# Optimization experiments

Hardware: AMD Instinct MI355X
Metric: run time of the kernel (lower is better)

The kernel has to match this reference:

```python
import jax, jax.numpy as jnp
import numpy as np


def exp_mix_frac(p1, p2, a1, b1, a2, b2):
    # stable merge of two (numerator, denominator) pairs carried in log-scale p
    p = jnp.maximum(p1, p2)
    e1 = jnp.exp(p1 - p)
    e2 = jnp.exp(p2 - p)
    return a1 * e1 + a2 * e2, b1 * e1 + b2 * e2, p


def assoc_reduce_step(left, right):
    akv_l, ak_l, w_l, p_l = left
    akv_r, ak_r, w_r, p_r = right
    a, b, p = exp_mix_frac(p_l + w_r, p_r, akv_l, ak_l, akv_r, ak_r)
    return a, b, w_l + w_r, p


def setup_inputs() -> dict:
    key = jax.random.key(0)
    ks = jax.random.split(key, 7)
    S, B, E = 2048, 8, 1024
    scale = 1.0 / np.sqrt(E)
    return {
        "x": jax.random.normal(ks[0], (S, B, E), jnp.float32),
        "tmrkv": jax.random.uniform(ks[1], (3 * E,), jnp.float32),
        "Wk": jax.random.normal(ks[2], (E, E), jnp.float32) * scale,
        "Wv": jax.random.normal(ks[3], (E, E), jnp.float32) * scale,
        "time_decay": jax.random.normal(ks[4], (E,), jnp.float32) - 1.0,
        "time_first": jax.random.normal(ks[5], (E,), jnp.float32),
        "Wout": jax.random.normal(ks[6], (E, E), jnp.float32) * scale,
    }


def reference(x, tmrkv, Wk, Wv, time_decay, time_first, Wout):
    # x: (S, B, E) time-major (batch_first=False path of the source module)
    S, B, E = x.shape
    x_prev = jnp.concatenate([jnp.zeros_like(x[:1]), x[:-1]], axis=0)
    # time_mix_rkv layout: [r | k | v]; r-branch is computed in the source but
    # never used in the associative-scan path, so it is omitted (same output).
    mk = tmrkv[E:2 * E]
    mv = tmrkv[2 * E:]
    k = (mk * x + (1.0 - mk) * x_prev) @ Wk  # (S, B, E)
    v = (mv * x + (1.0 - mv) * x_prev) @ Wv  # (S, B, E)

    k_ = k.reshape(S, B * E)
    v_ = v.reshape(S, B * E)
    W_ = jnp.broadcast_to(jnp.tile(time_decay, B)[None, :], (S, B * E))
    ones = jnp.ones_like(v_)
    # log-depth parallel scan over time with numerically-stable exp merge
    a_, b_, _, p_ = jax.lax.associative_scan(
        assoc_reduce_step, (v_, ones, W_, k_), axis=0)

    a_state = a_.reshape(S, B, E)
    b_state = b_.reshape(S, B, E)
    p_state = p_.reshape(S, B, E)
    c, d, _ = exp_mix_frac(p_state, k + time_first + time_decay,
                           a_state, b_state, v, jnp.ones_like(v))
    rwkv = c / d  # (S, B, E)
    return rwkv @ Wout
```

## Files before the change

### kernel.cpp

```cpp
#include <hip/hip_runtime.h>
#include <stdint.h>

#define S_LEN  2048
#define B_DIM  8
#define E_DIM  1024
#define BE     (B_DIM * E_DIM)
#define M_ROWS (S_LEN * B_DIM)
#define NCHUNK 64
#define CLEN   (S_LEN / NCHUNK)

typedef __attribute__((ext_vector_type(8))) short bf16x8;
typedef __attribute__((ext_vector_type(4))) float f32x4;

__device__ __forceinline__ unsigned short f2bf(float f) {
    unsigned int u = __float_as_uint(f);
    u += 0x7FFFu + ((u >> 16) & 1u);
    return (unsigned short)(u >> 16);
}
__device__ __forceinline__ float bf_lo(unsigned int u) {
    return __uint_as_float(u << 16);
}
__device__ __forceinline__ float bf_hi(unsigned int u) {
    return __uint_as_float(u & 0xFFFF0000u);
}

__global__ __launch_bounds__(256) void mix_kernel(
    const float* __restrict__ x, const float* __restrict__ tmrkv,
    unsigned short* __restrict__ xk, unsigned short* __restrict__ xv)
{
    int i = blockIdx.x * 256 + threadIdx.x;
    const float4* x4 = (const float4*)x;
    float4 xc = x4[i];
    float4 xp = make_float4(0.f, 0.f, 0.f, 0.f);
    if (i >= BE / 4) xp = x4[i - BE / 4];
    int e4 = i & (E_DIM / 4 - 1);
    float4 mk = ((const float4*)(tmrkv + E_DIM))[e4];
    float4 mv = ((const float4*)(tmrkv + 2 * E_DIM))[e4];
    ushort4 ok, ov;
    ok.x = f2bf(mk.x * xc.x + (1.f - mk.x) * xp.x);
    ok.y = f2bf(mk.y * xc.y + (1.f - mk.y) * xp.y);
    ok.z = f2bf(mk.z * xc.z + (1.f - mk.z) * xp.z);
    ok.w = f2bf(mk.w * xc.w + (1.f - mk.w) * xp.w);
    ov.x = f2bf(mv.x * xc.x + (1.f - mv.x) * xp.x);
    ov.y = f2bf(mv.y * xc.y + (1.f - mv.y) * xp.y);
    ov.z = f2bf(mv.z * xc.z + (1.f - mv.z) * xp.z);
    ov.w = f2bf(mv.w * xc.w + (1.f - mv.w) * xp.w);
    ((ushort4*)xk)[i] = ok;
    ((ushort4*)xv)[i] = ov;
}

__global__ __launch_bounds__(256) void cast_transpose_k(
    const float* __restrict__ w0, const float* __restrict__ w1,
    const float* __restrict__ w2,
    unsigned short* __restrict__ o0, unsigned short* __restrict__ o1,
    unsigned short* __restrict__ o2)
{
    const float* in = blockIdx.z == 0 ? w0 : (blockIdx.z == 1 ? w1 : w2);
    unsigned short* out = blockIdx.z == 0 ? o0 : (blockIdx.z == 1 ? o1 : o2);
    __shared__ float tile[32][33];
    int bx = blockIdx.x * 32, by = blockIdx.y * 32;
    int tx = threadIdx.x, ty = threadIdx.y;
    #pragma unroll
    for (int i = 0; i < 32; i += 8)
        tile[ty + i][tx] = in[(size_t)(by + ty + i) * E_DIM + bx + tx];
    __syncthreads();
    #pragma unroll
    for (int i = 0; i < 32; i += 8)
        out[(size_t)(bx + ty + i) * E_DIM + by + tx] = f2bf(tile[tx][ty + i]);
}

#define BM 128
#define BN 128
#define BK 64

template <typename OutT>
__global__ __launch_bounds__(256) void gemm_bf16_bt(
    const unsigned short* __restrict__ A,
    const unsigned short* __restrict__ BT,
    OutT* __restrict__ C, int M, int N, int K)
{
    __shared__ __align__(16) unsigned short As[BM * BK];
    __shared__ __align__(16) unsigned short Bs[BN * BK];
    const int tid  = threadIdx.x;
    const int wave = tid >> 6, lane = tid & 63;
    const int bm = blockIdx.x * BM, bn = blockIdx.y * BN;
    const int wr = (wave >> 1) * 64, wc = (wave & 1) * 64;
    const int lrow = lane & 15, lq = lane >> 4;

    f32x4 acc[4][4];
    #pragma unroll
    for (int i = 0; i < 4; ++i)
        #pragma unroll
        for (int j = 0; j < 4; ++j)
            acc[i][j] = (f32x4){0.f, 0.f, 0.f, 0.f};

    const int nk = K / BK;
    for (int kt = 0; kt < nk; ++kt) {
        __syncthreads();
        const int kk = kt * BK;
        #pragma unroll
        for (int s = 0; s < 4; ++s) {
            int idx = s * 256 + wave * 64 + lane;
            int r   = idx >> 3;
            int gc  = (idx & 7) ^ (r & 7);
            const char* ga = (const char*)(A  + (size_t)(bm + r) * K + kk) + gc * 16;
            const char* gb = (const char*)(BT + (size_t)(bn + r) * K + kk) + gc * 16;
            char* la = (char*)As + s * 4096 + wave * 1024;
            char* lb = (char*)Bs + s * 4096 + wave * 1024;
            __builtin_amdgcn_global_load_lds(
                (const __attribute__((address_space(1))) unsigned int*)ga,
                (__attribute__((address_space(3))) unsigned int*)la, 16, 0, 0);
            __builtin_amdgcn_global_load_lds(
                (const __attribute__((address_space(1))) unsigned int*)gb,
                (__attribute__((address_space(3))) unsigned int*)lb, 16, 0, 0);
        }
        __syncthreads();

        #pragma unroll
        for (int h = 0; h < 2; ++h) {
            bf16x8 af[4], bf[4];
            #pragma unroll
            for (int i = 0; i < 4; ++i) {
                int R = wr + i * 16 + lrow;
                af[i] = *(const bf16x8*)&As[R * BK + (((h << 2) | lq) ^ (R & 7)) * 8];
            }
            #pragma unroll
            for (int j = 0; j < 4; ++j) {
                int R = wc + j * 16 + lrow;
                bf[j] = *(const bf16x8*)&Bs[R * BK + (((h << 2) | lq) ^ (R & 7)) * 8];
            }
            #pragma unroll
            for (int i = 0; i < 4; ++i)
                #pragma unroll
                for (int j = 0; j < 4; ++j)
                    acc[i][j] = __builtin_amdgcn_mfma_f32_16x16x32_bf16(
                        af[i], bf[j], acc[i][j], 0, 0, 0);
        }
    }

    #pragma unroll
    for (int i = 0; i < 4; ++i)
        #pragma unroll
        for (int j = 0; j < 4; ++j)
            #pragma unroll
            for (int r = 0; r < 4; ++r) {
                int row = bm + wr + i * 16 + lq * 4 + r;
                int col = bn + wc + j * 16 + lrow;
                if constexpr (sizeof(OutT) == 2)
                    C[(size_t)row * N + col] = f2bf(acc[i][j][r]);
                else
                    C[(size_t)row * N + col] = acc[i][j][r];
            }
}

__device__ __forceinline__ void wkv_step(float& a, float& b, float& p,
                                         float kt, float vt, float w)
{
    float pw = p + w;
    float pn = fmaxf(pw, kt);
    float e1 = __expf(pw - pn), e2 = __expf(kt - pn);
    a = a * e1 + vt * e2;
    b = b * e1 + e2;
    p = pn;
}

__global__ __launch_bounds__(256) void scan_pass1(
    const unsigned int* __restrict__ k2, const unsigned int* __restrict__ v2,
    const float* __restrict__ tdec,
    float2* __restrict__ sA, float2* __restrict__ sB, float2* __restrict__ sP)
{
    int g   = blockIdx.x * 256 + threadIdx.x;
    int ch2 = g & (BE / 2 - 1);
    int c   = g >> 12;
    float2 w2 = ((const float2*)tdec)[ch2 & (E_DIM / 2 - 1)];
    size_t idx = (size_t)c * CLEN * (BE / 2) + ch2;
    unsigned int ku = k2[idx], vu = v2[idx];
    float a0 = bf_lo(vu), b0 = 1.f, p0 = bf_lo(ku);
    float a1 = bf_hi(vu), b1 = 1.f, p1 = bf_hi(ku);
    for (int j = 1; j < CLEN; ++j) {
        idx += BE / 2;
        ku = k2[idx]; vu = v2[idx];
        wkv_step(a0, b0, p0, bf_lo(ku), bf_lo(vu), w2.x);
        wkv_step(a1, b1, p1, bf_hi(ku), bf_hi(vu), w2.y);
    }
    sA[g] = make_float2(a0, a1);
    sB[g] = make_float2(b0, b1);
    sP[g] = make_float2(p0, p1);
}

__global__ __launch_bounds__(256) void scan_pass2(
    const float* __restrict__ tdec,
    float* __restrict__ sA, float* __restrict__ sB, float* __restrict__ sP)
{
    __shared__ float tA[64 * 65], tB[64 * 65], tP[64 * 65];
    const int t   = threadIdx.x;
    const int ch0 = blockIdx.x * 64;
    const int chl = t & 63;
    const int cq  = t >> 6;
    #pragma unroll 4
    for (int cc = 0; cc < 16; ++cc) {
        int c = cq * 16 + cc;
        int idx = c * BE + ch0 + chl;
        tA[chl * 65 + c] = sA[idx];
        tB[chl * 65 + c] = sB[idx];
        tP[chl * 65 + c] = sP[idx];
    }
    __syncthreads();
    const int lane = t & 63, wave = t >> 6;
    for (int i = 0; i < 16; ++i) {
        int ch = wave * 16 + i;
        float w = tdec[(ch0 + ch) & (E_DIM - 1)];
        float a = tA[ch * 65 + lane];
        float b = tB[ch * 65 + lane];
        float p = tP[ch * 65 + lane];
        float W = (float)CLEN * w;
        #pragma unroll
        for (int d = 1; d < 64; d <<= 1) {
            float a_l = __shfl_up(a, d);
            float b_l = __shfl_up(b, d);
            float p_l = __shfl_up(p, d);
            float W_l = __shfl_up(W, d);
            if (lane >= d) {
                float pw = p_l + W;
                float pn = fmaxf(pw, p);
                float e1 = __expf(pw - pn), e2 = __expf(p - pn);
                a = a_l * e1 + a * e2;
                b = b_l * e1 + b * e2;
                p = pn;
                W = W_l + W;
            }
        }
        float ea = __shfl_up(a, 1);
        float eb = __shfl_up(b, 1);
        float ep = __shfl_up(p, 1);
        if (lane == 0) { ea = 0.f; eb = 0.f; ep = -__builtin_inff(); }
        tA[ch * 65 + lane] = ea;
        tB[ch * 65 + lane] = eb;
        tP[ch * 65 + lane] = ep;
    }
    __syncthreads();
    #pragma unroll 4
    for (int cc = 0; cc < 16; ++cc) {
        int c = cq * 16 + cc;
        int idx = c * BE + ch0 + chl;
        sA[idx] = tA[chl * 65 + c];
        sB[idx] = tB[chl * 65 + c];
        sP[idx] = tP[chl * 65 + c];
    }
}

__global__ __launch_bounds__(256) void scan_pass3(
    const unsigned int* __restrict__ k2, const unsigned int* __restrict__ v2,
    const float* __restrict__ tdec, const float* __restrict__ tfir,
    const float2* __restrict__ sA, const float2* __restrict__ sB,
    const float2* __restrict__ sP, unsigned int* __restrict__ rwkv2)
{
    int g   = blockIdx.x * 256 + threadIdx.x;
    int ch2 = g & (BE / 2 - 1);
    int c   = g >> 12;
    int e2  = ch2 & (E_DIM / 2 - 1);
    float2 w2 = ((const float2*)tdec)[e2];
    float2 f2 = ((const float2*)tfir)[e2];
    float u20 = f2.x + w2.x, u21 = f2.y + w2.y;
    float2 av = sA[g], bv = sB[g], pv = sP[g];
    float a0 = av.x, b0 = bv.x, p0 = pv.x;
    float a1 = av.y, b1 = bv.y, p1 = pv.y;
    size_t idx = (size_t)c * CLEN * (BE / 2) + ch2;
    for (int j = 0; j < CLEN; ++j) {
        unsigned int ku = k2[idx], vu = v2[idx];
        float kt0 = bf_lo(ku), vt0 = bf_lo(vu);
        float kt1 = bf_hi(ku), vt1 = bf_hi(vu);
        wkv_step(a0, b0, p0, kt0, vt0, w2.x);
        wkv_step(a1, b1, p1, kt1, vt1, w2.y);
        float kb0 = kt0 + u20, kb1 = kt1 + u21;
        float q0 = fmaxf(p0, kb0), q1 = fmaxf(p1, kb1);
        float g0 = __expf(p0 - q0), h0 = __expf(kb0 - q0);
        float g1 = __expf(p1 - q1), h1 = __expf(kb1 - q1);
        float r0 = (a0 * g0 + vt0 * h0) / (b0 * g0 + h0);
        float r1 = (a1 * g1 + vt1 * h1) / (b1 * g1 + h1);
        rwkv2[idx] = (unsigned int)f2bf(r0) | ((unsigned int)f2bf(r1) << 16);
        idx += BE / 2;
    }
}

extern "C" void kernel_launch(void* const* d_in, const int* in_sizes, int n_in,
                              void* d_out, int out_size, void* d_ws, size_t ws_size,
                              hipStream_t stream)
{
    const float* x     = (const float*)d_in[0];
    const float* tmrkv = (const float*)d_in[1];
    const float* Wk    = (const float*)d_in[2];
    const float* Wv    = (const float*)d_in[3];
    const float* tdec  = (const float*)d_in[4];
    const float* tfir  = (const float*)d_in[5];
    const float* Wout  = (const float*)d_in[6];
    float* out = (float*)d_out;

    char* ws = (char*)d_ws;
    const size_t SZ_BF = (size_t)M_ROWS * E_DIM * 2;
    unsigned short* xk   = (unsigned short*)(ws);
    unsigned short* xv   = (unsigned short*)(ws + SZ_BF);
    unsigned short* kbuf = (unsigned short*)(ws + 2 * SZ_BF);
    unsigned short* vbuf = (unsigned short*)(ws + 3 * SZ_BF);
    unsigned short* WkT  = (unsigned short*)(ws + 4 * SZ_BF);
    unsigned short* WvT  = WkT + (size_t)E_DIM * E_DIM;
    unsigned short* WoutT= WvT + (size_t)E_DIM * E_DIM;
    float* sA = (float*)xv;
    float* sB = sA + (size_t)NCHUNK * BE;
    float* sP = sB + (size_t)NCHUNK * BE;
    unsigned short* rwkv = xk;

    mix_kernel<<<(M_ROWS * E_DIM / 4) / 256, 256, 0, stream>>>(x, tmrkv, xk, xv);

    dim3 tb(32, 8), tg(E_DIM / 32, E_DIM / 32, 3);
    cast_transpose_k<<<tg, tb, 0, stream>>>(Wk, Wv, Wout, WkT, WvT, WoutT);

    dim3 gg(M_ROWS / BM, E_DIM / BN);
    gemm_bf16_bt<unsigned short><<<gg, 256, 0, stream>>>(xk, WkT, kbuf,
                                                         M_ROWS, E_DIM, E_DIM);
    gemm_bf16_bt<unsigned short><<<gg, 256, 0, stream>>>(xv, WvT, vbuf,
                                                         M_ROWS, E_DIM, E_DIM);

    scan_pass1<<<(NCHUNK * BE / 2) / 256, 256, 0, stream>>>(
        (const unsigned int*)kbuf, (const unsigned int*)vbuf, tdec,
        (float2*)sA, (float2*)sB, (float2*)sP);
    scan_pass2<<<BE / 64, 256, 0, stream>>>(tdec, sA, sB, sP);
    scan_pass3<<<(NCHUNK * BE / 2) / 256, 256, 0, stream>>>(
        (const unsigned int*)kbuf, (const unsigned int*)vbuf, tdec, tfir,
        (const float2*)sA, (const float2*)sB, (const float2*)sP,
        (unsigned int*)rwkv);

    gemm_bf16_bt<float><<<gg, 256, 0, stream>>>(rwkv, WoutT, out,
                                                M_ROWS, E_DIM, E_DIM);
}
```

Measured before the change: 337.0 us.

## Double scan chunks, merge K/V GEMMs, single-exp merges, widen mix kernel

Raises the scan chunk count to 128, which shortens each thread's serial chain and doubles scan-pass parallelism. The chunk-level prefix in pass2 now handles two chunks per lane. The K and V GEMMs become one launch with a z-dimension, and the GEMM grid is reordered so N varies fastest. Each stable exp merge now uses one exp of -|d| plus selects instead of two exps, and the output division uses a fast reciprocal. The mix kernel processes 8 elements per thread and the scan loops are unrolled. The cost is larger scan-state buffers and a slightly less precise division.

Result: no change. 332.9 us (-1.2%).

```diff
diff --git a/kernel.cpp b/kernel.cpp
--- a/kernel.cpp
+++ b/kernel.cpp
@@ -6,8 +6,9 @@
 #define E_DIM  1024
 #define BE     (B_DIM * E_DIM)
 #define M_ROWS (S_LEN * B_DIM)
-#define NCHUNK 64
+#define NCHUNK 128
 #define CLEN   (S_LEN / NCHUNK)
+#define P_PER_T (BE / 2)
 
 typedef __attribute__((ext_vector_type(8))) short bf16x8;
 typedef __attribute__((ext_vector_type(4))) float f32x4;
@@ -30,23 +31,35 @@
 {
     int i = blockIdx.x * 256 + threadIdx.x;
     const float4* x4 = (const float4*)x;
-    float4 xc = x4[i];
-    float4 xp = make_float4(0.f, 0.f, 0.f, 0.f);
-    if (i >= BE / 4) xp = x4[i - BE / 4];
-    int e4 = i & (E_DIM / 4 - 1);
-    float4 mk = ((const float4*)(tmrkv + E_DIM))[e4];
-    float4 mv = ((const float4*)(tmrkv + 2 * E_DIM))[e4];
-    ushort4 ok, ov;
-    ok.x = f2bf(mk.x * xc.x + (1.f - mk.x) * xp.x);
-    ok.y = f2bf(mk.y * xc.y + (1.f - mk.y) * xp.y);
-    ok.z = f2bf(mk.z * xc.z + (1.f - mk.z) * xp.z);
-    ok.w = f2bf(mk.w * xc.w + (1.f - mk.w) * xp.w);
-    ov.x = f2bf(mv.x * xc.x + (1.f - mv.x) * xp.x);
-    ov.y = f2bf(mv.y * xc.y + (1.f - mv.y) * xp.y);
-    ov.z = f2bf(mv.z * xc.z + (1.f - mv.z) * xp.z);
-    ov.w = f2bf(mv.w * xc.w + (1.f - mv.w) * xp.w);
-    ((ushort4*)xk)[i] = ok;
-    ((ushort4*)xv)[i] = ov;
+    float4 xc[2], xp[2];
+    xc[0] = x4[2 * i];
+    xc[1] = x4[2 * i + 1];
+    if (i >= BE / 8) {
+        xp[0] = x4[2 * i - BE / 4];
+        xp[1] = x4[2 * i + 1 - BE / 4];
+    } else {
+        xp[0] = make_float4(0.f, 0.f, 0.f, 0.f);
+        xp[1] = make_float4(0.f, 0.f, 0.f, 0.f);
+    }
+    int e4 = (2 * i) & (E_DIM / 4 - 1);
+    ushort4 ok[2], ov[2];
+    #pragma unroll
+    for (int h = 0; h < 2; ++h) {
+        float4 mk = ((const float4*)(tmrkv + E_DIM))[e4 + h];
+        float4 mv = ((const float4*)(tmrkv + 2 * E_DIM))[e4 + h];
+        ok[h].x = f2bf(mk.x * xc[h].x + (1.f - mk.x) * xp[h].x);
+        ok[h].y = f2bf(mk.y * xc[h].y + (1.f - mk.y) * xp[h].y);
+        ok[h].z = f2bf(mk.z * xc[h].z + (1.f - mk.z) * xp[h].z);
+        ok[h].w = f2bf(mk.w * xc[h].w + (1.f - mk.w) * xp[h].w);
+        ov[h].x = f2bf(mv.x * xc[h].x + (1.f - mv.x) * xp[h].x);
+        ov[h].y = f2bf(mv.y * xc[h].y + (1.f - mv.y) * xp[h].y);
+        ov[h].z = f2bf(mv.z * xc[h].z + (1.f - mv.z) * xp[h].z);
+        ov[h].w = f2bf(mv.w * xc[h].w + (1.f - mv.w) * xp[h].w);
+    }
+    ((ushort4*)xk)[2 * i]     = ok[0];
+    ((ushort4*)xk)[2 * i + 1] = ok[1];
+    ((ushort4*)xv)[2 * i]     = ov[0];
+    ((ushort4*)xv)[2 * i + 1] = ov[1];
 }
 
 __global__ __launch_bounds__(256) void cast_transpose_k(
@@ -74,7 +87,7 @@
 #define BK 64
 
 template <typename OutT>
-__global__ __launch_bounds__(256) void gemm_bf16_bt(
+__device__ __forceinline__ void gemm_body(
     const unsigned short* __restrict__ A,
     const unsigned short* __restrict__ BT,
     OutT* __restrict__ C, int M, int N, int K)
@@ -83,7 +96,7 @@
     __shared__ __align__(16) unsigned short Bs[BN * BK];
     const int tid  = threadIdx.x;
     const int wave = tid >> 6, lane = tid & 63;
-    const int bm = blockIdx.x * BM, bn = blockIdx.y * BN;
+    const int bm = blockIdx.y * BM, bn = blockIdx.x * BN;
     const int wr = (wave >> 1) * 64, wc = (wave & 1) * 64;
     const int lrow = lane & 15, lq = lane >> 4;
 
@@ -153,15 +166,50 @@
             }
 }
 
+__global__ __launch_bounds__(256) void gemm_kv(
+    const unsigned short* __restrict__ A0, const unsigned short* __restrict__ B0,
+    unsigned short* __restrict__ C0,
+    const unsigned short* __restrict__ A1, const unsigned short* __restrict__ B1,
+    unsigned short* __restrict__ C1, int M, int N, int K)
+{
+    if (blockIdx.z == 0) gemm_body<unsigned short>(A0, B0, C0, M, N, K);
+    else                 gemm_body<unsigned short>(A1, B1, C1, M, N, K);
+}
+
+__global__ __launch_bounds__(256) void gemm_out(
+    const unsigned short* __restrict__ A, const unsigned short* __restrict__ BT,
+    float* __restrict__ C, int M, int N, int K)
+{
+    gemm_body<float>(A, BT, C, M, N, K);
+}
+
 __device__ __forceinline__ void wkv_step(float& a, float& b, float& p,
                                          float kt, float vt, float w)
 {
     float pw = p + w;
-    float pn = fmaxf(pw, kt);
-    float e1 = __expf(pw - pn), e2 = __expf(kt - pn);
+    float d  = kt - pw;
+    float em = __expf(-fabsf(d));
+    bool  c  = d > 0.f;
+    float e1 = c ? em : 1.f;
+    float e2 = c ? 1.f : em;
     a = a * e1 + vt * e2;
     b = b * e1 + e2;
-    p = pn;
+    p = fmaxf(pw, kt);
+}
+
+__device__ __forceinline__ void wkv_combine(float& la, float& lb, float& lp,
+                                            float ra, float rb, float rp,
+                                            float Wr)
+{
+    float pw = lp + Wr;
+    float d  = rp - pw;
+    float em = __expf(-fabsf(d));
+    bool  c  = d > 0.f;
+    float e1 = c ? em : 1.f;
+    float e2 = c ? 1.f : em;
+    la = la * e1 + ra * e2;
+    lb = lb * e1 + rb * e2;
+    lp = fmaxf(pw, rp);
 }
 
 __global__ __launch_bounds__(256) void scan_pass1(
@@ -169,16 +217,17 @@
     const float* __restrict__ tdec,
     float2* __restrict__ sA, float2* __restrict__ sB, float2* __restrict__ sP)
 {
-    int g   = blockIdx.x * 256 + threadIdx.x;
-    int ch2 = g & (BE / 2 - 1);
-    int c   = g >> 12;
-    float2 w2 = ((const float2*)tdec)[ch2 & (E_DIM / 2 - 1)];
-    size_t idx = (size_t)c * CLEN * (BE / 2) + ch2;
+    int g  = blockIdx.x * 256 + threadIdx.x;
+    int pr = g & (P_PER_T - 1);
+    int c  = g >> 12;
+    float2 w2 = ((const float2*)tdec)[pr & (E_DIM / 2 - 1)];
+    size_t idx = (size_t)c * CLEN * P_PER_T + pr;
     unsigned int ku = k2[idx], vu = v2[idx];
     float a0 = bf_lo(vu), b0 = 1.f, p0 = bf_lo(ku);
     float a1 = bf_hi(vu), b1 = 1.f, p1 = bf_hi(ku);
+    #pragma unroll
     for (int j = 1; j < CLEN; ++j) {
-        idx += BE / 2;
+        idx += P_PER_T;
         ku = k2[idx]; vu = v2[idx];
         wkv_step(a0, b0, p0, bf_lo(ku), bf_lo(vu), w2.x);
         wkv_step(a1, b1, p1, bf_hi(ku), bf_hi(vu), w2.y);
@@ -192,28 +241,31 @@
     const float* __restrict__ tdec,
     float* __restrict__ sA, float* __restrict__ sB, float* __restrict__ sP)
 {
-    __shared__ float tA[64 * 65], tB[64 * 65], tP[64 * 65];
+    __shared__ float tA[32 * 130], tB[32 * 130], tP[32 * 130];
     const int t   = threadIdx.x;
-    const int ch0 = blockIdx.x * 64;
-    const int chl = t & 63;
-    const int cq  = t >> 6;
+    const int ch0 = blockIdx.x * 32;
+    const int chl = t & 31;
+    const int cq  = t >> 5;
     #pragma unroll 4
     for (int cc = 0; cc < 16; ++cc) {
         int c = cq * 16 + cc;
         int idx = c * BE + ch0 + chl;
-        tA[chl * 65 + c] = sA[idx];
-        tB[chl * 65 + c] = sB[idx];
-        tP[chl * 65 + c] = sP[idx];
+        tA[chl * 130 + c] = sA[idx];
+        tB[chl * 130 + c] = sB[idx];
+        tP[chl * 130 + c] = sP[idx];
     }
     __syncthreads();
     const int lane = t & 63, wave = t >> 6;
-    for (int i = 0; i < 16; ++i) {
-        int ch = wave * 16 + i;
-        float w = tdec[(ch0 + ch) & (E_DIM - 1)];
-        float a = tA[ch * 65 + lane];
-        float b = tB[ch * 65 + lane];
-        float p = tP[ch * 65 + lane];
-        float W = (float)CLEN * w;
+    for (int i = 0; i < 8; ++i) {
+        int ch = wave * 8 + i;
+        float w  = tdec[(ch0 + ch) & (E_DIM - 1)];
+        float Lw = (float)CLEN * w;
+        int c0 = 2 * lane, c1 = 2 * lane + 1;
+        float a0 = tA[ch * 130 + c0], b0 = tB[ch * 130 + c0], p0 = tP[ch * 130 + c0];
+        float a1 = tA[ch * 130 + c1], b1 = tB[ch * 130 + c1], p1 = tP[ch * 130 + c1];
+        float a = a0, b = b0, p = p0;
+        wkv_combine(a, b, p, a1, b1, p1, Lw);
+        float W = 2.f * Lw;
         #pragma unroll
         for (int d = 1; d < 64; d <<= 1) {
             float a_l = __shfl_up(a, d);
@@ -221,12 +273,9 @@
             float p_l = __shfl_up(p, d);
             float W_l = __shfl_up(W, d);
             if (lane >= d) {
-                float pw = p_l + W;
-                float pn = fmaxf(pw, p);
-                float e1 = __expf(pw - pn), e2 = __expf(p - pn);
-                a = a_l * e1 + a * e2;
-                b = b_l * e1 + b * e2;
-                p = pn;
+                float na = a_l, nb = b_l, np = p_l;
+                wkv_combine(na, nb, np, a, b, p, W);
+                a = na; b = nb; p = np;
                 W = W_l + W;
             }
         }
@@ -234,18 +283,22 @@
         float eb = __shfl_up(b, 1);
         float ep = __shfl_up(p, 1);
         if (lane == 0) { ea = 0.f; eb = 0.f; ep = -__builtin_inff(); }
-        tA[ch * 65 + lane] = ea;
-        tB[ch * 65 + lane] = eb;
-        tP[ch * 65 + lane] = ep;
+        tA[ch * 130 + c0] = ea;
+        tB[ch * 130 + c0] = eb;
+        tP[ch * 130 + c0] = ep;
+        wkv_combine(ea, eb, ep, a0, b0, p0, Lw);
+        tA[ch * 130 + c1] = ea;
+        tB[ch * 130 + c1] = eb;
+        tP[ch * 130 + c1] = ep;
     }
     __syncthreads();
     #pragma unroll 4
     for (int cc = 0; cc < 16; ++cc) {
         int c = cq * 16 + cc;
         int idx = c * BE + ch0 + chl;
-        sA[idx] = tA[chl * 65 + c];
-        sB[idx] = tB[chl * 65 + c];
-        sP[idx] = tP[chl * 65 + c];
+        sA[idx] = tA[chl * 130 + c];
+        sB[idx] = tB[chl * 130 + c];
+        sP[idx] = tP[chl * 130 + c];
     }
 }
 
@@ -255,31 +308,36 @@
     const float2* __restrict__ sA, const float2* __restrict__ sB,
     const float2* __restrict__ sP, unsigned int* __restrict__ rwkv2)
 {
-    int g   = blockIdx.x * 256 + threadIdx.x;
-    int ch2 = g & (BE / 2 - 1);
-    int c   = g >> 12;
-    int e2  = ch2 & (E_DIM / 2 - 1);
-    float2 w2 = ((const float2*)tdec)[e2];
-    float2 f2 = ((const float2*)tfir)[e2];
-    float u20 = f2.x + w2.x, u21 = f2.y + w2.y;
+    int g  = blockIdx.x * 256 + threadIdx.x;
+    int pr = g & (P_PER_T - 1);
+    int c  = g >> 12;
+    int e2i = pr & (E_DIM / 2 - 1);
+    float2 w2 = ((const float2*)tdec)[e2i];
+    float2 f2 = ((const float2*)tfir)[e2i];
+    float u0 = f2.x + w2.x, u1 = f2.y + w2.y;
     float2 av = sA[g], bv = sB[g], pv = sP[g];
     float a0 = av.x, b0 = bv.x, p0 = pv.x;
     float a1 = av.y, b1 = bv.y, p1 = pv.y;
-    size_t idx = (size_t)c * CLEN * (BE / 2) + ch2;
+    size_t idx = (size_t)c * CLEN * P_PER_T + pr;
+    #pragma unroll
     for (int j = 0; j < CLEN; ++j) {
         unsigned int ku = k2[idx], vu = v2[idx];
         float kt0 = bf_lo(ku), vt0 = bf_lo(vu);
         float kt1 = bf_hi(ku), vt1 = bf_hi(vu);
         wkv_step(a0, b0, p0, kt0, vt0, w2.x);
         wkv_step(a1, b1, p1, kt1, vt1, w2.y);
-        float kb0 = kt0 + u20, kb1 = kt1 + u21;
-        float q0 = fmaxf(p0, kb0), q1 = fmaxf(p1, kb1);
-        float g0 = __expf(p0 - q0), h0 = __expf(kb0 - q0);
-        float g1 = __expf(p1 - q1), h1 = __expf(kb1 - q1);
-        float r0 = (a0 * g0 + vt0 * h0) / (b0 * g0 + h0);
-        float r1 = (a1 * g1 + vt1 * h1) / (b1 * g1 + h1);
+        float kb0 = kt0 + u0, kb1 = kt1 + u1;
+        float d0 = kb0 - p0, d1 = kb1 - p1;
+        float m0 = __expf(-fabsf(d0)), m1 = __expf(-fabsf(d1));
+        bool  c0 = d0 > 0.f, c1 = d1 > 0.f;
+        float f10 = c0 ? m0 : 1.f, f20 = c0 ? 1.f : m0;
+        float f11 = c1 ? m1 : 1.f, f21 = c1 ? 1.f : m1;
+        float n0 = a0 * f10 + vt0 * f20, de0 = b0 * f10 + f20;
+        float n1 = a1 * f11 + vt1 * f21, de1 = b1 * f11 + f21;
+        float r0 = n0 * __builtin_amdgcn_rcpf(de0);
+        float r1 = n1 * __builtin_amdgcn_rcpf(de1);
         rwkv2[idx] = (unsigned int)f2bf(r0) | ((unsigned int)f2bf(r1) << 16);
-        idx += BE / 2;
+        idx += P_PER_T;
     }
 }
 
@@ -310,26 +368,24 @@
     float* sP = sB + (size_t)NCHUNK * BE;
     unsigned short* rwkv = xk;
 
-    mix_kernel<<<(M_ROWS * E_DIM / 4) / 256, 256, 0, stream>>>(x, tmrkv, xk, xv);
+    mix_kernel<<<(M_ROWS * E_DIM / 8) / 256, 256, 0, stream>>>(x, tmrkv, xk, xv);
 
     dim3 tb(32, 8), tg(E_DIM / 32, E_DIM / 32, 3);
     cast_transpose_k<<<tg, tb, 0, stream>>>(Wk, Wv, Wout, WkT, WvT, WoutT);
 
-    dim3 gg(M_ROWS / BM, E_DIM / BN);
-    gemm_bf16_bt<unsigned short><<<gg, 256, 0, stream>>>(xk, WkT, kbuf,
-                                                         M_ROWS, E_DIM, E_DIM);
-    gemm_bf16_bt<unsigned short><<<gg, 256, 0, stream>>>(xv, WvT, vbuf,
-                                                         M_ROWS, E_DIM, E_DIM);
-
-    scan_pass1<<<(NCHUNK * BE / 2) / 256, 256, 0, stream>>>(
+    dim3 gkv(E_DIM / BN, M_ROWS / BM, 2);
+    gemm_kv<<<gkv, 256, 0, stream>>>(xk, WkT, kbuf, xv, WvT, vbuf,
+                                     M_ROWS, E_DIM, E_DIM);
+
+    scan_pass1<<<(NCHUNK * P_PER_T) / 256, 256, 0, stream>>>(
         (const unsigned int*)kbuf, (const unsigned int*)vbuf, tdec,
         (float2*)sA, (float2*)sB, (float2*)sP);
-    scan_pass2<<<BE / 64, 256, 0, stream>>>(tdec, sA, sB, sP);
-    scan_pass3<<<(NCHUNK * BE / 2) / 256, 256, 0, stream>>>(
+    scan_pass2<<<BE / 32, 256, 0, stream>>>(tdec, sA, sB, sP);
+    scan_pass3<<<(NCHUNK * P_PER_T) / 256, 256, 0, stream>>>(
         (const unsigned int*)kbuf, (const unsigned int*)vbuf, tdec, tfir,
         (const float2*)sA, (const float2*)sB, (const float2*)sP,
         (unsigned int*)rwkv);
 
-    gemm_bf16_bt<float><<<gg, 256, 0, stream>>>(rwkv, WoutT, out,
-                                                M_ROWS, E_DIM, E_DIM);
-}
+    dim3 gg(E_DIM / BN, M_ROWS / BM);
+    gemm_out<<<gg, 256, 0, stream>>>(rwkv, WoutT, out, M_ROWS, E_DIM, E_DIM);
+}
```
